# Performance work log

Measured on AMD Instinct MI355X. Metric: run time of the kernel, lower is better.

## Reference

```python
import jax, jax.numpy as jnp
import numpy as np
from jax import lax

VOCAB, EMBED, HIDDEN = 32000, 512, 1024
BATCH, SEQ = 64, 512


def setup_inputs() -> dict:
    key = jax.random.key(0)
    ks = jax.random.split(key, 10)
    H, E, V = HIDDEN, EMBED, VOCAB
    s = lambda *d: 1.0 / np.sqrt(d[0])
    return {
        "x": jax.random.randint(ks[0], (BATCH, SEQ), 0, V, dtype=jnp.int32),
        "embed_table": jax.random.normal(ks[1], (V, E), jnp.float32) * 0.02,
        "Wx0": jax.random.normal(ks[2], (E, 4 * H), jnp.float32) * s(E),
        "Wh0": jax.random.normal(ks[3], (H, 4 * H), jnp.float32) * s(H),
        "b0": jnp.zeros((4 * H,), jnp.float32),
        "Wx1": jax.random.normal(ks[4], (H, 4 * H), jnp.float32) * s(H),
        "Wh1": jax.random.normal(ks[5], (H, 4 * H), jnp.float32) * s(H),
        "b1": jnp.zeros((4 * H,), jnp.float32),
        "Wout": jax.random.normal(ks[6], (H, V), jnp.float32) * s(H),
        "bout": jnp.zeros((V,), jnp.float32),
    }


def _lstm_layer(inp, Wx, Wh, b):
    # inp: [B, S, D_in] -> hidden states [B, S, H]
    B = inp.shape[0]
    H = Wh.shape[0]
    # Precompute the input projection for all timesteps (one big GEMM).
    x4 = jnp.einsum("bsd,dg->bsg", inp, Wx) + b           # [B, S, 4H]
    x4 = jnp.swapaxes(x4, 0, 1)                              # [S, B, 4H]
    h0 = jnp.zeros((B, H), inp.dtype)
    c0 = jnp.zeros((B, H), inp.dtype)

    def step(carry, xt4):
        h, c = carry
        g = xt4 + h @ Wh                                     # [B, 4H]
        i, f, gg, o = jnp.split(g, 4, axis=-1)
        c = jax.nn.sigmoid(f) * c + jax.nn.sigmoid(i) * jnp.tanh(gg)
        h = jax.nn.sigmoid(o) * jnp.tanh(c)
        return (h, c), h

    _, hs = lax.scan(step, (h0, c0), x4)                     # hs: [S, B, H]
    return jnp.swapaxes(hs, 0, 1)                            # [B, S, H]


def reference(x, embed_table, Wx0, Wh0, b0, Wx1, Wh1, b1, Wout, bout):
    emb = embed_table[x]                                      # [B, S, E]
    h1 = _lstm_layer(emb, Wx0, Wh0, b0)                       # [B, S, H]
    h2 = _lstm_layer(h1, Wx1, Wh1, b1)                        # [B, S, H]
    logits = h2[:, -1, :] @ Wout + bout                       # [B, V] (last timestep)
    return jax.nn.softmax(logits, axis=-1)
```

## Files before the change

### kernel.cpp

```cpp
#include <hip/hip_runtime.h>


#define BB 64
#define SS 512
#define EE 512
#define HH 1024
#define GG 4096
#define VV 32000

using bf16x8 = __attribute__((ext_vector_type(8))) __bf16;
using f32x4  = __attribute__((ext_vector_type(4))) float;

__device__ __forceinline__ unsigned short f2bf(float f) {
    unsigned u = __float_as_uint(f);
    unsigned r = u + 0x7FFFu + ((u >> 16) & 1u);
    return (unsigned short)(r >> 16);
}
__device__ __forceinline__ float bf2f(unsigned short u) {
    return __uint_as_float(((unsigned)u) << 16);
}
__device__ __forceinline__ float sigm(float x) {
    return 1.0f / (1.0f + expf(-x));
}
__device__ __forceinline__ bf16x8 ld_frag_coh(const unsigned long long* p) {
    union { unsigned long long u[2]; bf16x8 v; } x;
    x.u[0] = __hip_atomic_load(p,     __ATOMIC_RELAXED, __HIP_MEMORY_SCOPE_AGENT);
    x.u[1] = __hip_atomic_load(p + 1, __ATOMIC_RELAXED, __HIP_MEMORY_SCOPE_AGENT);
    return x.v;
}
__device__ __forceinline__ void gate_poll(const unsigned int* p, unsigned tgt) {
    while (__hip_atomic_load(p, __ATOMIC_RELAXED, __HIP_MEMORY_SCOPE_AGENT) < tgt)
        __builtin_amdgcn_s_sleep(1);
    __builtin_amdgcn_sched_barrier(0);
}

__global__ void pack_b(const float* __restrict__ B, unsigned short* __restrict__ out,
                       int KT, int N) {
    int bid = blockIdx.x;
    int lane = threadIdx.x;
    int nt = bid / KT, kt = bid % KT;
    int k = kt * 32 + ((lane >> 4) << 3);
    int n = nt * 16 + (lane & 15);
    size_t base = ((size_t)bid * 64 + lane) * 8;
    #pragma unroll
    for (int j = 0; j < 8; ++j)
        out[base + j] = f2bf(B[(size_t)(k + j) * N + n]);
}

__global__ void pack_wh(const float* __restrict__ Wh, unsigned short* __restrict__ out) {
    int f = blockIdx.x;
    int lane = threadIdx.x;
    int kt = f & 31, nt = (f >> 5) & 1, g = f >> 6;
    int nloc = lane & 15;
    int q = nt * 2 + (nloc >> 3), cj = nloc & 7;
    int gcol = q * HH + 8 * g + cj;
    int k = kt * 32 + ((lane >> 4) << 3);
    size_t base = ((size_t)f * 64 + lane) * 8;
    #pragma unroll
    for (int j = 0; j < 8; ++j)
        out[base + j] = f2bf(Wh[(size_t)(k + j) * GG + gcol]);
}

__global__ void embed_pack(const int* __restrict__ x, const float* __restrict__ tab,
                           unsigned short* __restrict__ out) {
    int bid = blockIdx.x;
    int lane = threadIdx.x;
    int mt = bid >> 4, kt = bid & 15;
    int m = mt * 16 + (lane & 15);
    int idx = x[(m & 63) * SS + (m >> 6)];
    int kb = kt * 32 + ((lane >> 4) << 3);
    size_t base = ((size_t)bid * 64 + lane) * 8;
    const float* src = tab + (size_t)idx * EE + kb;
    #pragma unroll
    for (int j = 0; j < 8; ++j)
        out[base + j] = f2bf(src[j]);
}

template<int MODE>
__global__ __launch_bounds__(256) void gemm_bias(
    const unsigned short* __restrict__ Ap, const unsigned short* __restrict__ Bp,
    const float* __restrict__ bias, void* __restrict__ Cout, int N, int KT) {
    __shared__ unsigned short tile[64][72];
    const int tid = threadIdx.x, lane = tid & 63, w = tid >> 6;
    const int ntg = blockIdx.x * 4 + w;
    const int m0t = blockIdx.y * 4;
    const bf16x8* Av = reinterpret_cast<const bf16x8*>(Ap);
    const bf16x8* Bv = reinterpret_cast<const bf16x8*>(Bp);
    f32x4 acc[4] = {{0.f,0.f,0.f,0.f},{0.f,0.f,0.f,0.f},{0.f,0.f,0.f,0.f},{0.f,0.f,0.f,0.f}};
    for (int kt = 0; kt < KT; ++kt) {
        bf16x8 b = Bv[((size_t)ntg * KT + kt) * 64 + lane];
        #pragma unroll
        for (int mt = 0; mt < 4; ++mt) {
            bf16x8 a = Av[((size_t)(m0t + mt) * KT + kt) * 64 + lane];
            acc[mt] = __builtin_amdgcn_mfma_f32_16x16x32_bf16(a, b, acc[mt], 0, 0, 0);
        }
    }
    const int col = ntg * 16 + (lane & 15);
    const int rq = (lane >> 4) << 2;
    const float bb = bias[col];
    if (MODE == 0) {
        #pragma unroll
        for (int mt = 0; mt < 4; ++mt)
            #pragma unroll
            for (int i = 0; i < 4; ++i) {
                int row = (m0t + mt) * 16 + rq + i;
                ((float*)Cout)[(size_t)row * N + col] = acc[mt][i] + bb;
            }
    } else {
        const int cl = w * 16 + (lane & 15);
        #pragma unroll
        for (int mt = 0; mt < 4; ++mt)
            #pragma unroll
            for (int i = 0; i < 4; ++i)
                tile[cl][mt * 16 + rq + i] = f2bf(acc[mt][i] + bb);
        __syncthreads();
        const int c = tid >> 2, b0 = (tid & 3) << 4;
        unsigned short* dst = (unsigned short*)Cout +
            ((size_t)blockIdx.y * GG + (size_t)blockIdx.x * 64) * 64 + (size_t)tid * 16;
        const uint4* s4 = reinterpret_cast<const uint4*>(&tile[c][b0]);
        reinterpret_cast<uint4*>(dst)[0] = s4[0];
        reinterpret_cast<uint4*>(dst)[1] = s4[1];
    }
}

__global__ void zero_init(unsigned short* __restrict__ h0a,
                          unsigned short* __restrict__ h0b,
                          unsigned int* __restrict__ flags) {
    int i = blockIdx.x * 256 + threadIdx.x;
    for (int k = i; k < BB * HH; k += 64 * 256) { h0a[k] = 0; h0b[k] = 0; }
    for (int k = i; k < 9216; k += 64 * 256) flags[k] = 0;
}

__global__ __launch_bounds__(256, 2) void lstm_fused(
    const unsigned short* __restrict__ x4s,
    const unsigned short* __restrict__ wh0p, const unsigned short* __restrict__ wh1p,
    const unsigned short* __restrict__ wx1p,
    const float* __restrict__ b1,
    unsigned short* __restrict__ hb0, unsigned short* __restrict__ hb1,
    unsigned short* __restrict__ hb2, unsigned short* __restrict__ hb3,
    unsigned int* __restrict__ flags) {
    __shared__ float gx[2][32][36];
    __shared__ __align__(16) unsigned short hlds[32][8];
    __shared__ __align__(16) unsigned short Blds[64 * 64 * 8];
    const int tid = threadIdx.x, lane = tid & 63, w = tid >> 6;
    const int L = (blockIdx.x >= 256) ? 1 : 0;
    const int inner = blockIdx.x & 255;
    const int g = inner >> 1, hf = inner & 1;
    unsigned int* done   = flags + L * 4096 + hf * 2048;
    unsigned int* go_own = flags + 8192 + (L * 2 + hf) * 256;
    unsigned int* go_oth = flags + 8192 + ((1 - L) * 2 + hf) * 256;
    const int rep = (g & 15) * 16;

    {
        const uint4* src = reinterpret_cast<const uint4*>(L ? wh1p : wh0p) + (size_t)g * 4096;
        uint4* dst = reinterpret_cast<uint4*>(Blds);
        #pragma unroll
        for (int i = 0; i < 16; ++i)
            dst[i * 256 + tid] = src[i * 256 + tid];
    }
    __syncthreads();
    const bf16x8* Bl = reinterpret_cast<const bf16x8*>(Blds);
    const bf16x8* Wx = reinterpret_cast<const bf16x8*>(wx1p);

    const int msub = w & 1, kh = w >> 1;
    const int kh16 = kh * 16;
    const int nloc = lane & 15;
    const int cj = nloc & 7;
    const int q0 = nloc >> 3;
    const int gq0 = q0 * HH + 8 * g + cj;
    const int gq1 = (2 + q0) * HH + 8 * g + cj;
    const int rbase = msub * 16 + ((lane >> 4) << 2);
    const size_t afrag_base = ((size_t)(2 * hf + msub) * 32 + (size_t)kh * 16) * 64 + lane;
    const int row_l = tid >> 3, cj2 = tid & 7;
    float c = 0.f;

    if (L == 0) {
        ushort4 xv0 = {0, 0, 0, 0}, xv1 = {0, 0, 0, 0};
        if (kh == 0) {
            xv0 = *reinterpret_cast<const ushort4*>(x4s + ((size_t)gq0) * 64 + 32 * hf + rbase);
            xv1 = *reinterpret_cast<const ushort4*>(x4s + ((size_t)gq1) * 64 + 32 * hf + rbase);
        }
        #pragma unroll 1
        for (int t = 0; t < SS; ++t) {
            if (t > 0) {
                gate_poll(&go_own[rep], (unsigned)t);
                if (t >= 2) gate_poll(&go_oth[rep], (unsigned)(t - 1));
            }
            const unsigned long long* hv =
                reinterpret_cast<const unsigned long long*>((t & 1) ? hb1 : hb0);
            unsigned short* hout = (t & 1) ? hb0 : hb1;

            bf16x8 A[16];
            #pragma unroll
            for (int k = 0; k < 16; ++k)
                A[k] = ld_frag_coh(hv + (afrag_base + (size_t)k * 64) * 2);

            f32x4 acc0 = {0.f, 0.f, 0.f, 0.f}, acc1 = {0.f, 0.f, 0.f, 0.f};
            #pragma unroll
            for (int k = 0; k < 16; ++k) {
                acc0 = __builtin_amdgcn_mfma_f32_16x16x32_bf16(
                    A[k], Bl[(kh16 + k) * 64 + lane], acc0, 0, 0, 0);
                acc1 = __builtin_amdgcn_mfma_f32_16x16x32_bf16(
                    A[k], Bl[(32 + kh16 + k) * 64 + lane], acc1, 0, 0, 0);
            }
            if (kh == 0) {
                gx[0][nloc][rbase + 0] = acc0[0] + bf2f(xv0.x);
                gx[0][nloc][rbase + 1] = acc0[1] + bf2f(xv0.y);
                gx[0][nloc][rbase + 2] = acc0[2] + bf2f(xv0.z);
                gx[0][nloc][rbase + 3] = acc0[3] + bf2f(xv0.w);
                gx[0][16 + nloc][rbase + 0] = acc1[0] + bf2f(xv1.x);
                gx[0][16 + nloc][rbase + 1] = acc1[1] + bf2f(xv1.y);
                gx[0][16 + nloc][rbase + 2] = acc1[2] + bf2f(xv1.z);
                gx[0][16 + nloc][rbase + 3] = acc1[3] + bf2f(xv1.w);
            } else {
                gx[1][nloc][rbase + 0] = acc0[0];
                gx[1][nloc][rbase + 1] = acc0[1];
                gx[1][nloc][rbase + 2] = acc0[2];
                gx[1][nloc][rbase + 3] = acc0[3];
                gx[1][16 + nloc][rbase + 0] = acc1[0];
                gx[1][16 + nloc][rbase + 1] = acc1[1];
                gx[1][16 + nloc][rbase + 2] = acc1[2];
                gx[1][16 + nloc][rbase + 3] = acc1[3];
            }
            __syncthreads();

            float gi = gx[0][0 * 8 + cj2][row_l] + gx[1][0 * 8 + cj2][row_l];
            float gf = gx[0][1 * 8 + cj2][row_l] + gx[1][1 * 8 + cj2][row_l];
            float gg = gx[0][2 * 8 + cj2][row_l] + gx[1][2 * 8 + cj2][row_l];
            float go = gx[0][3 * 8 + cj2][row_l] + gx[1][3 * 8 + cj2][row_l];
            float cn = sigm(gf) * c + sigm(gi) * tanhf(gg);
            c = cn;
            hlds[row_l][cj2] = f2bf(sigm(go) * tanhf(cn));
            __syncthreads();

            if (tid < 32) {
                union { uint4 v; unsigned long long u[2]; } cv;
                cv.v = *reinterpret_cast<const uint4*>(&hlds[tid][0]);
                const int m = 32 * hf + tid;
                unsigned long long* dst = reinterpret_cast<unsigned long long*>(
                    hout + (((size_t)(m >> 4) * 32 + (g >> 2)) * 64 + (g & 3) * 16 + (m & 15)) * 8);
                __hip_atomic_store(dst,     cv.u[0], __ATOMIC_RELAXED, __HIP_MEMORY_SCOPE_AGENT);
                __hip_atomic_store(dst + 1, cv.u[1], __ATOMIC_RELAXED, __HIP_MEMORY_SCOPE_AGENT);
            }
            if (w == 0)
                asm volatile("s_waitcnt vmcnt(0)" ::: "memory");
            if (tid == 0)
                __hip_atomic_store(&done[g * 16], (unsigned)(t + 1),
                                   __ATOMIC_RELAXED, __HIP_MEMORY_SCOPE_AGENT);
            if (kh == 0 && t + 1 < SS) {
                xv0 = *reinterpret_cast<const ushort4*>(
                    x4s + ((size_t)(t + 1) * GG + gq0) * 64 + 32 * hf + rbase);
                xv1 = *reinterpret_cast<const ushort4*>(
                    x4s + ((size_t)(t + 1) * GG + gq1) * 64 + 32 * hf + rbase);
            }
            if (g == 0 && tid < 64) {
                const unsigned tgt = (unsigned)(t + 1);
                unsigned v0 = 0, v1 = 0;
                while (1) {
                    if (v0 < tgt)
                        v0 = __hip_atomic_load(&done[tid * 16], __ATOMIC_RELAXED,
                                               __HIP_MEMORY_SCOPE_AGENT);
                    if (v1 < tgt)
                        v1 = __hip_atomic_load(&done[(tid + 64) * 16], __ATOMIC_RELAXED,
                                               __HIP_MEMORY_SCOPE_AGENT);
                    if (__all((v0 >= tgt) && (v1 >= tgt))) break;
                    __builtin_amdgcn_s_sleep(1);
                }
                if (tid < 16)
                    __hip_atomic_store(&go_own[tid * 16], tgt, __ATOMIC_RELAXED,
                                       __HIP_MEMORY_SCOPE_AGENT);
            }
        }
    } else {
        const float bb0 = b1[gq0], bb1 = b1[gq1];
        #pragma unroll 1
        for (int t = 0; t < SS; ++t) {
            gate_poll(&go_oth[rep], (unsigned)(t + 1));
            const unsigned long long* hv1 =
                reinterpret_cast<const unsigned long long*>((t & 1) ? hb0 : hb1);
            bf16x8 A1[16];
            #pragma unroll
            for (int k = 0; k < 16; ++k)
                A1[k] = ld_frag_coh(hv1 + (afrag_base + (size_t)k * 64) * 2);

            if (t > 0)
                gate_poll(&go_own[rep], (unsigned)t);
            const unsigned long long* hv2 =
                reinterpret_cast<const unsigned long long*>((t & 1) ? hb3 : hb2);
            unsigned short* hout2 = (t & 1) ? hb2 : hb3;
            bf16x8 A2[16];
            #pragma unroll
            for (int k = 0; k < 16; ++k)
                A2[k] = ld_frag_coh(hv2 + (afrag_base + (size_t)k * 64) * 2);

            f32x4 acc0 = {0.f, 0.f, 0.f, 0.f}, acc1 = {0.f, 0.f, 0.f, 0.f};
            {
                bf16x8 BXa[8], BXb[8];
                #pragma unroll
                for (int j = 0; j < 8; ++j) {
                    BXa[j] = Wx[((size_t)(g * 64 + kh16 + j)) * 64 + lane];
                    BXb[j] = Wx[((size_t)(g * 64 + 32 + kh16 + j)) * 64 + lane];
                }
                #pragma unroll
                for (int j = 0; j < 8; ++j) {
                    acc0 = __builtin_amdgcn_mfma_f32_16x16x32_bf16(A1[j], BXa[j], acc0, 0, 0, 0);
                    acc1 = __builtin_amdgcn_mfma_f32_16x16x32_bf16(A1[j], BXb[j], acc1, 0, 0, 0);
                }
                #pragma unroll
                for (int j = 0; j < 8; ++j) {
                    BXa[j] = Wx[((size_t)(g * 64 + kh16 + 8 + j)) * 64 + lane];
                    BXb[j] = Wx[((size_t)(g * 64 + 32 + kh16 + 8 + j)) * 64 + lane];
                }
                #pragma unroll
                for (int j = 0; j < 8; ++j) {
                    acc0 = __builtin_amdgcn_mfma_f32_16x16x32_bf16(A1[8 + j], BXa[j], acc0, 0, 0, 0);
                    acc1 = __builtin_amdgcn_mfma_f32_16x16x32_bf16(A1[8 + j], BXb[j], acc1, 0, 0, 0);
                }
            }
            #pragma unroll
            for (int k = 0; k < 16; ++k) {
                acc0 = __builtin_amdgcn_mfma_f32_16x16x32_bf16(
                    A2[k], Bl[(kh16 + k) * 64 + lane], acc0, 0, 0, 0);
                acc1 = __builtin_amdgcn_mfma_f32_16x16x32_bf16(
                    A2[k], Bl[(32 + kh16 + k) * 64 + lane], acc1, 0, 0, 0);
            }

            if (kh == 0) {
                gx[0][nloc][rbase + 0] = acc0[0] + bb0;
                gx[0][nloc][rbase + 1] = acc0[1] + bb0;
                gx[0][nloc][rbase + 2] = acc0[2] + bb0;
                gx[0][nloc][rbase + 3] = acc0[3] + bb0;
                gx[0][16 + nloc][rbase + 0] = acc1[0] + bb1;
                gx[0][16 + nloc][rbase + 1] = acc1[1] + bb1;
                gx[0][16 + nloc][rbase + 2] = acc1[2] + bb1;
                gx[0][16 + nloc][rbase + 3] = acc1[3] + bb1;
            } else {
                gx[1][nloc][rbase + 0] = acc0[0];
                gx[1][nloc][rbase + 1] = acc0[1];
                gx[1][nloc][rbase + 2] = acc0[2];
                gx[1][nloc][rbase + 3] = acc0[3];
                gx[1][16 + nloc][rbase + 0] = acc1[0];
                gx[1][16 + nloc][rbase + 1] = acc1[1];
                gx[1][16 + nloc][rbase + 2] = acc1[2];
                gx[1][16 + nloc][rbase + 3] = acc1[3];
            }
            __syncthreads();

            float gi = gx[0][0 * 8 + cj2][row_l] + gx[1][0 * 8 + cj2][row_l];
            float gf = gx[0][1 * 8 + cj2][row_l] + gx[1][1 * 8 + cj2][row_l];
            float gg = gx[0][2 * 8 + cj2][row_l] + gx[1][2 * 8 + cj2][row_l];
            float go = gx[0][3 * 8 + cj2][row_l] + gx[1][3 * 8 + cj2][row_l];
            float cn = sigm(gf) * c + sigm(gi) * tanhf(gg);
            c = cn;
            hlds[row_l][cj2] = f2bf(sigm(go) * tanhf(cn));
            __syncthreads();

            if (tid < 32) {
                union { uint4 v; unsigned long long u[2]; } cv;
                cv.v = *reinterpret_cast<const uint4*>(&hlds[tid][0]);
                const int m = 32 * hf + tid;
                unsigned long long* dst = reinterpret_cast<unsigned long long*>(
                    hout2 + (((size_t)(m >> 4) * 32 + (g >> 2)) * 64 + (g & 3) * 16 + (m & 15)) * 8);
                __hip_atomic_store(dst,     cv.u[0], __ATOMIC_RELAXED, __HIP_MEMORY_SCOPE_AGENT);
                __hip_atomic_store(dst + 1, cv.u[1], __ATOMIC_RELAXED, __HIP_MEMORY_SCOPE_AGENT);
            }
            if (w == 0)
                asm volatile("s_waitcnt vmcnt(0)" ::: "memory");
            if (tid == 0)
                __hip_atomic_store(&done[g * 16], (unsigned)(t + 1),
                                   __ATOMIC_RELAXED, __HIP_MEMORY_SCOPE_AGENT);
            if (g == 0 && tid < 64) {
                const unsigned tgt = (unsigned)(t + 1);
                unsigned v0 = 0, v1 = 0;
                while (1) {
                    if (v0 < tgt)
                        v0 = __hip_atomic_load(&done[tid * 16], __ATOMIC_RELAXED,
                                               __HIP_MEMORY_SCOPE_AGENT);
                    if (v1 < tgt)
                        v1 = __hip_atomic_load(&done[(tid + 64) * 16], __ATOMIC_RELAXED,
                                               __HIP_MEMORY_SCOPE_AGENT);
                    if (__all((v0 >= tgt) && (v1 >= tgt))) break;
                    __builtin_amdgcn_s_sleep(1);
                }
                if (tid < 16)
                    __hip_atomic_store(&go_own[tid * 16], tgt, __ATOMIC_RELAXED,
                                       __HIP_MEMORY_SCOPE_AGENT);
            }
        }
    }
}

__global__ __launch_bounds__(256) void softmax_rows(const float* __restrict__ logits,
                                                    float* __restrict__ out) {
    __shared__ float red[256];
    int rr = blockIdx.x, tid = threadIdx.x;
    const float* L = logits + (size_t)rr * VV;
    float m = -1e30f;
    for (int i = tid; i < VV; i += 256) m = fmaxf(m, L[i]);
    red[tid] = m; __syncthreads();
    for (int s = 128; s > 0; s >>= 1) { if (tid < s) red[tid] = fmaxf(red[tid], red[tid + s]); __syncthreads(); }
    m = red[0]; __syncthreads();
    float sum = 0.f;
    for (int i = tid; i < VV; i += 256) sum += expf(L[i] - m);
    red[tid] = sum; __syncthreads();
    for (int s = 128; s > 0; s >>= 1) { if (tid < s) red[tid] += red[tid + s]; __syncthreads(); }
    float inv = 1.f / red[0];
    for (int i = tid; i < VV; i += 256) out[(size_t)rr * VV + i] = expf(L[i] - m) * inv;
}

extern "C" void kernel_launch(void* const* d_in, const int* in_sizes, int n_in,
                              void* d_out, int out_size, void* d_ws, size_t ws_size,
                              hipStream_t stream) {
    const int*   x    = (const int*)  d_in[0];
    const float* tab  = (const float*)d_in[1];
    const float* Wx0  = (const float*)d_in[2];
    const float* Wh0  = (const float*)d_in[3];
    const float* b0   = (const float*)d_in[4];
    const float* Wx1  = (const float*)d_in[5];
    const float* Wh1  = (const float*)d_in[6];
    const float* b1   = (const float*)d_in[7];
    const float* Wout = (const float*)d_in[8];
    const float* bout = (const float*)d_in[9];
    float* out = (float*)d_out;

    unsigned short* ws    = (unsigned short*)d_ws;
    unsigned short* embA  = ws;
    unsigned short* wx0p  = embA  + 16777216;
    unsigned short* wh0p  = wx0p  + 2097152;
    unsigned short* wx1p  = wh0p  + 4194304;
    unsigned short* wh1p  = wx1p  + 4194304;
    unsigned short* woutp = wh1p  + 4194304;
    unsigned short* x4s   = woutp + 32768000;
    unsigned short* h1A   = x4s   + 134217728;
    unsigned short* hb0   = h1A   + 33554432;
    unsigned short* hb1   = hb0   + 65536;
    unsigned short* hb2   = hb1   + 65536;
    unsigned short* hb3   = hb2   + 65536;
    float* logits = (float*)(hb3 + 65536);
    unsigned int* flags = (unsigned int*)(logits + 2048000);

    pack_b <<<256 * 16, 64, 0, stream>>>(Wx0, wx0p, 16, GG);
    pack_wh<<<8192, 64, 0, stream>>>(Wh0, wh0p);
    pack_wh<<<8192, 64, 0, stream>>>(Wx1, wx1p);
    pack_wh<<<8192, 64, 0, stream>>>(Wh1, wh1p);
    pack_b <<<2000 * 32, 64, 0, stream>>>(Wout, woutp, 32, VV);

    zero_init<<<64, 256, 0, stream>>>(hb0, hb2, flags);

    embed_pack<<<32768, 64, 0, stream>>>(x, tab, embA);
    gemm_bias<1><<<dim3(GG / 64, 32768 / 64), 256, 0, stream>>>(embA, wx0p, b0, x4s, GG, EE / 32);

    {
        const unsigned short* a0 = x4s;
        const unsigned short* a1 = wh0p; const unsigned short* a2 = wh1p;
        const unsigned short* a3 = wx1p; const float* a4 = b1;
        unsigned short *a5 = hb0, *a6 = hb1, *a7 = hb2, *a8 = hb3;
        unsigned int* a9 = flags;
        void* args[] = {&a0, &a1, &a2, &a3, &a4, &a5, &a6, &a7, &a8, &a9};
        hipLaunchCooperativeKernel((const void*)lstm_fused, dim3(512), dim3(256),
                                   args, 0, stream);
    }

    gemm_bias<0><<<dim3(VV / 64, 1), 256, 0, stream>>>(hb2, woutp, bout, logits, VV, HH / 32);
    softmax_rows<<<64, 256, 0, stream>>>(logits, out);
}
```

Before: 3.885 ms.

## Fuse layer-0 input projection into the recurrent LSTM kernel

Drops the separate large embedding x Wx0 GEMM and its bf16 x4s intermediate buffer. Each layer-0 block now computes its slice of the input projection per timestep inside the fused recurrent kernel, before polling for the previous hidden state. The embedding fragments for the next step are prefetched after publishing h. Wx0 is repacked into the recurrent gate layout to make this possible. This removes a large global-memory write and reread, but adds MFMA work and Wx0 global loads on every step of the serial recurrence. Hiding that work relies on it overlapping with the wait on the barrier.

```diff
diff --git a/kernel.cpp b/kernel.cpp
--- a/kernel.cpp
+++ b/kernel.cpp
@@ -47,10 +47,12 @@
         out[base + j] = f2bf(B[(size_t)(k + j) * N + n]);
 }
 
-__global__ void pack_wh(const float* __restrict__ Wh, unsigned short* __restrict__ out) {
+__global__ void pack_whk(const float* __restrict__ W, unsigned short* __restrict__ out,
+                         int KT) {
     int f = blockIdx.x;
     int lane = threadIdx.x;
-    int kt = f & 31, nt = (f >> 5) & 1, g = f >> 6;
+    int kt = f % KT, r = f / KT;
+    int nt = r & 1, g = r >> 1;
     int nloc = lane & 15;
     int q = nt * 2 + (nloc >> 3), cj = nloc & 7;
     int gcol = q * HH + 8 * g + cj;
@@ -58,7 +60,7 @@
     size_t base = ((size_t)f * 64 + lane) * 8;
     #pragma unroll
     for (int j = 0; j < 8; ++j)
-        out[base + j] = f2bf(Wh[(size_t)(k + j) * GG + gcol]);
+        out[base + j] = f2bf(W[(size_t)(k + j) * GG + gcol]);
 }
 
 __global__ void embed_pack(const int* __restrict__ x, const float* __restrict__ tab,
@@ -76,11 +78,9 @@
         out[base + j] = f2bf(src[j]);
 }
 
-template<int MODE>
 __global__ __launch_bounds__(256) void gemm_bias(
     const unsigned short* __restrict__ Ap, const unsigned short* __restrict__ Bp,
-    const float* __restrict__ bias, void* __restrict__ Cout, int N, int KT) {
-    __shared__ unsigned short tile[64][72];
+    const float* __restrict__ bias, float* __restrict__ Cout, int N, int KT) {
     const int tid = threadIdx.x, lane = tid & 63, w = tid >> 6;
     const int ntg = blockIdx.x * 4 + w;
     const int m0t = blockIdx.y * 4;
@@ -98,29 +98,13 @@
     const int col = ntg * 16 + (lane & 15);
     const int rq = (lane >> 4) << 2;
     const float bb = bias[col];
-    if (MODE == 0) {
+    #pragma unroll
+    for (int mt = 0; mt < 4; ++mt)
         #pragma unroll
-        for (int mt = 0; mt < 4; ++mt)
-            #pragma unroll
-            for (int i = 0; i < 4; ++i) {
-                int row = (m0t + mt) * 16 + rq + i;
-                ((float*)Cout)[(size_t)row * N + col] = acc[mt][i] + bb;
-            }
-    } else {
-        const int cl = w * 16 + (lane & 15);
-        #pragma unroll
-        for (int mt = 0; mt < 4; ++mt)
-            #pragma unroll
-            for (int i = 0; i < 4; ++i)
-                tile[cl][mt * 16 + rq + i] = f2bf(acc[mt][i] + bb);
-        __syncthreads();
-        const int c = tid >> 2, b0 = (tid & 3) << 4;
-        unsigned short* dst = (unsigned short*)Cout +
-            ((size_t)blockIdx.y * GG + (size_t)blockIdx.x * 64) * 64 + (size_t)tid * 16;
-        const uint4* s4 = reinterpret_cast<const uint4*>(&tile[c][b0]);
-        reinterpret_cast<uint4*>(dst)[0] = s4[0];
-        reinterpret_cast<uint4*>(dst)[1] = s4[1];
-    }
+        for (int i = 0; i < 4; ++i) {
+            int row = (m0t + mt) * 16 + rq + i;
+            Cout[(size_t)row * N + col] = acc[mt][i] + bb;
+        }
 }
 
 __global__ void zero_init(unsigned short* __restrict__ h0a,
@@ -132,10 +116,11 @@
 }
 
 __global__ __launch_bounds__(256, 2) void lstm_fused(
-    const unsigned short* __restrict__ x4s,
+    const unsigned short* __restrict__ embA,
+    const unsigned short* __restrict__ wx0p,
     const unsigned short* __restrict__ wh0p, const unsigned short* __restrict__ wh1p,
     const unsigned short* __restrict__ wx1p,
-    const float* __restrict__ b1,
+    const float* __restrict__ b0c, const float* __restrict__ b1c,
     unsigned short* __restrict__ hb0, unsigned short* __restrict__ hb1,
     unsigned short* __restrict__ hb2, unsigned short* __restrict__ hb3,
     unsigned int* __restrict__ flags) {
@@ -160,7 +145,6 @@
     }
     __syncthreads();
     const bf16x8* Bl = reinterpret_cast<const bf16x8*>(Blds);
-    const bf16x8* Wx = reinterpret_cast<const bf16x8*>(wx1p);
 
     const int msub = w & 1, kh = w >> 1;
     const int kh16 = kh * 16;
@@ -175,13 +159,27 @@
     float c = 0.f;
 
     if (L == 0) {
-        ushort4 xv0 = {0, 0, 0, 0}, xv1 = {0, 0, 0, 0};
-        if (kh == 0) {
-            xv0 = *reinterpret_cast<const ushort4*>(x4s + ((size_t)gq0) * 64 + 32 * hf + rbase);
-            xv1 = *reinterpret_cast<const ushort4*>(x4s + ((size_t)gq1) * 64 + 32 * hf + rbase);
+        const float bb0 = b0c[gq0], bb1 = b0c[gq1];
+        const bf16x8* Wx0v = reinterpret_cast<const bf16x8*>(wx0p);
+        const bf16x8* Ev   = reinterpret_cast<const bf16x8*>(embA);
+        const int kh8 = kh * 8;
+        bf16x8 Ae[8];
+        {
+            const int mt = 2 * hf + msub;
+            #pragma unroll
+            for (int j = 0; j < 8; ++j)
+                Ae[j] = Ev[((size_t)(mt * 16 + kh8 + j)) * 64 + lane];
         }
         #pragma unroll 1
         for (int t = 0; t < SS; ++t) {
+            f32x4 acc0 = {0.f, 0.f, 0.f, 0.f}, acc1 = {0.f, 0.f, 0.f, 0.f};
+            #pragma unroll
+            for (int j = 0; j < 8; ++j) {
+                bf16x8 BXa = Wx0v[((size_t)(g * 32 + kh8 + j)) * 64 + lane];
+                bf16x8 BXb = Wx0v[((size_t)(g * 32 + 16 + kh8 + j)) * 64 + lane];
+                acc0 = __builtin_amdgcn_mfma_f32_16x16x32_bf16(Ae[j], BXa, acc0, 0, 0, 0);
+                acc1 = __builtin_amdgcn_mfma_f32_16x16x32_bf16(Ae[j], BXb, acc1, 0, 0, 0);
+            }
             if (t > 0) {
                 gate_poll(&go_own[rep], (unsigned)t);
                 if (t >= 2) gate_poll(&go_oth[rep], (unsigned)(t - 1));
@@ -195,7 +193,6 @@
             for (int k = 0; k < 16; ++k)
                 A[k] = ld_frag_coh(hv + (afrag_base + (size_t)k * 64) * 2);
 
-            f32x4 acc0 = {0.f, 0.f, 0.f, 0.f}, acc1 = {0.f, 0.f, 0.f, 0.f};
             #pragma unroll
             for (int k = 0; k < 16; ++k) {
                 acc0 = __builtin_amdgcn_mfma_f32_16x16x32_bf16(
@@ -203,128 +200,6 @@
                 acc1 = __builtin_amdgcn_mfma_f32_16x16x32_bf16(
                     A[k], Bl[(32 + kh16 + k) * 64 + lane], acc1, 0, 0, 0);
             }
-            if (kh == 0) {
-                gx[0][nloc][rbase + 0] = acc0[0] + bf2f(xv0.x);
-                gx[0][nloc][rbase + 1] = acc0[1] + bf2f(xv0.y);
-                gx[0][nloc][rbase + 2] = acc0[2] + bf2f(xv0.z);
-                gx[0][nloc][rbase + 3] = acc0[3] + bf2f(xv0.w);
-                gx[0][16 + nloc][rbase + 0] = acc1[0] + bf2f(xv1.x);
-                gx[0][16 + nloc][rbase + 1] = acc1[1] + bf2f(xv1.y);
-                gx[0][16 + nloc][rbase + 2] = acc1[2] + bf2f(xv1.z);
-                gx[0][16 + nloc][rbase + 3] = acc1[3] + bf2f(xv1.w);
-            } else {
-                gx[1][nloc][rbase + 0] = acc0[0];
-                gx[1][nloc][rbase + 1] = acc0[1];
-                gx[1][nloc][rbase + 2] = acc0[2];
-                gx[1][nloc][rbase + 3] = acc0[3];
-                gx[1][16 + nloc][rbase + 0] = acc1[0];
-                gx[1][16 + nloc][rbase + 1] = acc1[1];
-                gx[1][16 + nloc][rbase + 2] = acc1[2];
-                gx[1][16 + nloc][rbase + 3] = acc1[3];
-            }
-            __syncthreads();
-
-            float gi = gx[0][0 * 8 + cj2][row_l] + gx[1][0 * 8 + cj2][row_l];
-            float gf = gx[0][1 * 8 + cj2][row_l] + gx[1][1 * 8 + cj2][row_l];
-            float gg = gx[0][2 * 8 + cj2][row_l] + gx[1][2 * 8 + cj2][row_l];
-            float go = gx[0][3 * 8 + cj2][row_l] + gx[1][3 * 8 + cj2][row_l];
-            float cn = sigm(gf) * c + sigm(gi) * tanhf(gg);
-            c = cn;
-            hlds[row_l][cj2] = f2bf(sigm(go) * tanhf(cn));
-            __syncthreads();
-
-            if (tid < 32) {
-                union { uint4 v; unsigned long long u[2]; } cv;
-                cv.v = *reinterpret_cast<const uint4*>(&hlds[tid][0]);
-                const int m = 32 * hf + tid;
-                unsigned long long* dst = reinterpret_cast<unsigned long long*>(
-                    hout + (((size_t)(m >> 4) * 32 + (g >> 2)) * 64 + (g & 3) * 16 + (m & 15)) * 8);
-                __hip_atomic_store(dst,     cv.u[0], __ATOMIC_RELAXED, __HIP_MEMORY_SCOPE_AGENT);
-                __hip_atomic_store(dst + 1, cv.u[1], __ATOMIC_RELAXED, __HIP_MEMORY_SCOPE_AGENT);
-            }
-            if (w == 0)
-                asm volatile("s_waitcnt vmcnt(0)" ::: "memory");
-            if (tid == 0)
-                __hip_atomic_store(&done[g * 16], (unsigned)(t + 1),
-                                   __ATOMIC_RELAXED, __HIP_MEMORY_SCOPE_AGENT);
-            if (kh == 0 && t + 1 < SS) {
-                xv0 = *reinterpret_cast<const ushort4*>(
-                    x4s + ((size_t)(t + 1) * GG + gq0) * 64 + 32 * hf + rbase);
-                xv1 = *reinterpret_cast<const ushort4*>(
-                    x4s + ((size_t)(t + 1) * GG + gq1) * 64 + 32 * hf + rbase);
-            }
-            if (g == 0 && tid < 64) {
-                const unsigned tgt = (unsigned)(t + 1);
-                unsigned v0 = 0, v1 = 0;
-                while (1) {
-                    if (v0 < tgt)
-                        v0 = __hip_atomic_load(&done[tid * 16], __ATOMIC_RELAXED,
-                                               __HIP_MEMORY_SCOPE_AGENT);
-                    if (v1 < tgt)
-                        v1 = __hip_atomic_load(&done[(tid + 64) * 16], __ATOMIC_RELAXED,
-                                               __HIP_MEMORY_SCOPE_AGENT);
-                    if (__all((v0 >= tgt) && (v1 >= tgt))) break;
-                    __builtin_amdgcn_s_sleep(1);
-                }
-                if (tid < 16)
-                    __hip_atomic_store(&go_own[tid * 16], tgt, __ATOMIC_RELAXED,
-                                       __HIP_MEMORY_SCOPE_AGENT);
-            }
-        }
-    } else {
-        const float bb0 = b1[gq0], bb1 = b1[gq1];
-        #pragma unroll 1
-        for (int t = 0; t < SS; ++t) {
-            gate_poll(&go_oth[rep], (unsigned)(t + 1));
-            const unsigned long long* hv1 =
-                reinterpret_cast<const unsigned long long*>((t & 1) ? hb0 : hb1);
-            bf16x8 A1[16];
-            #pragma unroll
-            for (int k = 0; k < 16; ++k)
-                A1[k] = ld_frag_coh(hv1 + (afrag_base + (size_t)k * 64) * 2);
-
-            if (t > 0)
-                gate_poll(&go_own[rep], (unsigned)t);
-            const unsigned long long* hv2 =
-                reinterpret_cast<const unsigned long long*>((t & 1) ? hb3 : hb2);
-            unsigned short* hout2 = (t & 1) ? hb2 : hb3;
-            bf16x8 A2[16];
-            #pragma unroll
-            for (int k = 0; k < 16; ++k)
-                A2[k] = ld_frag_coh(hv2 + (afrag_base + (size_t)k * 64) * 2);
-
-            f32x4 acc0 = {0.f, 0.f, 0.f, 0.f}, acc1 = {0.f, 0.f, 0.f, 0.f};
-            {
-                bf16x8 BXa[8], BXb[8];
-                #pragma unroll
-                for (int j = 0; j < 8; ++j) {
-                    BXa[j] = Wx[((size_t)(g * 64 + kh16 + j)) * 64 + lane];
-                    BXb[j] = Wx[((size_t)(g * 64 + 32 + kh16 + j)) * 64 + lane];
-                }
-                #pragma unroll
-                for (int j = 0; j < 8; ++j) {
-                    acc0 = __builtin_amdgcn_mfma_f32_16x16x32_bf16(A1[j], BXa[j], acc0, 0, 0, 0);
-                    acc1 = __builtin_amdgcn_mfma_f32_16x16x32_bf16(A1[j], BXb[j], acc1, 0, 0, 0);
-                }
-                #pragma unroll
-                for (int j = 0; j < 8; ++j) {
-                    BXa[j] = Wx[((size_t)(g * 64 + kh16 + 8 + j)) * 64 + lane];
-                    BXb[j] = Wx[((size_t)(g * 64 + 32 + kh16 + 8 + j)) * 64 + lane];
-                }
-                #pragma unroll
-                for (int j = 0; j < 8; ++j) {
-                    acc0 = __builtin_amdgcn_mfma_f32_16x16x32_bf16(A1[8 + j], BXa[j], acc0, 0, 0, 0);
-                    acc1 = __builtin_amdgcn_mfma_f32_16x16x32_bf16(A1[8 + j], BXb[j], acc1, 0, 0, 0);
-                }
-            }
-            #pragma unroll
-            for (int k = 0; k < 16; ++k) {
-                acc0 = __builtin_amdgcn_mfma_f32_16x16x32_bf16(
-                    A2[k], Bl[(kh16 + k) * 64 + lane], acc0, 0, 0, 0);
-                acc1 = __builtin_amdgcn_mfma_f32_16x16x32_bf16(
-                    A2[k], Bl[(32 + kh16 + k) * 64 + lane], acc1, 0, 0, 0);
-            }
-
             if (kh == 0) {
                 gx[0][nloc][rbase + 0] = acc0[0] + bb0;
                 gx[0][nloc][rbase + 1] = acc0[1] + bb0;
@@ -360,6 +235,129 @@
                 cv.v = *reinterpret_cast<const uint4*>(&hlds[tid][0]);
                 const int m = 32 * hf + tid;
                 unsigned long long* dst = reinterpret_cast<unsigned long long*>(
+                    hout + (((size_t)(m >> 4) * 32 + (g >> 2)) * 64 + (g & 3) * 16 + (m & 15)) * 8);
+                __hip_atomic_store(dst,     cv.u[0], __ATOMIC_RELAXED, __HIP_MEMORY_SCOPE_AGENT);
+                __hip_atomic_store(dst + 1, cv.u[1], __ATOMIC_RELAXED, __HIP_MEMORY_SCOPE_AGENT);
+            }
+            if (w == 0)
+                asm volatile("s_waitcnt vmcnt(0)" ::: "memory");
+            if (tid == 0)
+                __hip_atomic_store(&done[g * 16], (unsigned)(t + 1),
+                                   __ATOMIC_RELAXED, __HIP_MEMORY_SCOPE_AGENT);
+            if (t + 1 < SS) {
+                const int mt1 = 4 * (t + 1) + 2 * hf + msub;
+                #pragma unroll
+                for (int j = 0; j < 8; ++j)
+                    Ae[j] = Ev[((size_t)(mt1 * 16 + kh8 + j)) * 64 + lane];
+            }
+            if (g == 0 && tid < 64) {
+                const unsigned tgt = (unsigned)(t + 1);
+                unsigned v0 = 0, v1 = 0;
+                while (1) {
+                    if (v0 < tgt)
+                        v0 = __hip_atomic_load(&done[tid * 16], __ATOMIC_RELAXED,
+                                               __HIP_MEMORY_SCOPE_AGENT);
+                    if (v1 < tgt)
+                        v1 = __hip_atomic_load(&done[(tid + 64) * 16], __ATOMIC_RELAXED,
+                                               __HIP_MEMORY_SCOPE_AGENT);
+                    if (__all((v0 >= tgt) && (v1 >= tgt))) break;
+                    __builtin_amdgcn_s_sleep(1);
+                }
+                if (tid < 16)
+                    __hip_atomic_store(&go_own[tid * 16], tgt, __ATOMIC_RELAXED,
+                                       __HIP_MEMORY_SCOPE_AGENT);
+            }
+        }
+    } else {
+        const float bb0 = b1c[gq0], bb1 = b1c[gq1];
+        const bf16x8* Wx = reinterpret_cast<const bf16x8*>(wx1p);
+        #pragma unroll 1
+        for (int t = 0; t < SS; ++t) {
+            gate_poll(&go_oth[rep], (unsigned)(t + 1));
+            const unsigned long long* hv1 =
+                reinterpret_cast<const unsigned long long*>((t & 1) ? hb0 : hb1);
+            bf16x8 A1[16];
+            #pragma unroll
+            for (int k = 0; k < 16; ++k)
+                A1[k] = ld_frag_coh(hv1 + (afrag_base + (size_t)k * 64) * 2);
+
+            if (t > 0)
+                gate_poll(&go_own[rep], (unsigned)t);
+            const unsigned long long* hv2 =
+                reinterpret_cast<const unsigned long long*>((t & 1) ? hb3 : hb2);
+            unsigned short* hout2 = (t & 1) ? hb2 : hb3;
+            bf16x8 A2[16];
+            #pragma unroll
+            for (int k = 0; k < 16; ++k)
+                A2[k] = ld_frag_coh(hv2 + (afrag_base + (size_t)k * 64) * 2);
+
+            f32x4 acc0 = {0.f, 0.f, 0.f, 0.f}, acc1 = {0.f, 0.f, 0.f, 0.f};
+            {
+                bf16x8 BXa[8], BXb[8];
+                #pragma unroll
+                for (int j = 0; j < 8; ++j) {
+                    BXa[j] = Wx[((size_t)(g * 64 + kh16 + j)) * 64 + lane];
+                    BXb[j] = Wx[((size_t)(g * 64 + 32 + kh16 + j)) * 64 + lane];
+                }
+                #pragma unroll
+                for (int j = 0; j < 8; ++j) {
+                    acc0 = __builtin_amdgcn_mfma_f32_16x16x32_bf16(A1[j], BXa[j], acc0, 0, 0, 0);
+                    acc1 = __builtin_amdgcn_mfma_f32_16x16x32_bf16(A1[j], BXb[j], acc1, 0, 0, 0);
+                }
+                #pragma unroll
+                for (int j = 0; j < 8; ++j) {
+                    BXa[j] = Wx[((size_t)(g * 64 + kh16 + 8 + j)) * 64 + lane];
+                    BXb[j] = Wx[((size_t)(g * 64 + 32 + kh16 + 8 + j)) * 64 + lane];
+                }
+                #pragma unroll
+                for (int j = 0; j < 8; ++j) {
+                    acc0 = __builtin_amdgcn_mfma_f32_16x16x32_bf16(A1[8 + j], BXa[j], acc0, 0, 0, 0);
+                    acc1 = __builtin_amdgcn_mfma_f32_16x16x32_bf16(A1[8 + j], BXb[j], acc1, 0, 0, 0);
+                }
+            }
+            #pragma unroll
+            for (int k = 0; k < 16; ++k) {
+                acc0 = __builtin_amdgcn_mfma_f32_16x16x32_bf16(
+                    A2[k], Bl[(kh16 + k) * 64 + lane], acc0, 0, 0, 0);
+                acc1 = __builtin_amdgcn_mfma_f32_16x16x32_bf16(
+                    A2[k], Bl[(32 + kh16 + k) * 64 + lane], acc1, 0, 0, 0);
+            }
+
+            if (kh == 0) {
+                gx[0][nloc][rbase + 0] = acc0[0] + bb0;
+                gx[0][nloc][rbase + 1] = acc0[1] + bb0;
+                gx[0][nloc][rbase + 2] = acc0[2] + bb0;
+                gx[0][nloc][rbase + 3] = acc0[3] + bb0;
+                gx[0][16 + nloc][rbase + 0] = acc1[0] + bb1;
+                gx[0][16 + nloc][rbase + 1] = acc1[1] + bb1;
+                gx[0][16 + nloc][rbase + 2] = acc1[2] + bb1;
+                gx[0][16 + nloc][rbase + 3] = acc1[3] + bb1;
+            } else {
+                gx[1][nloc][rbase + 0] = acc0[0];
+                gx[1][nloc][rbase + 1] = acc0[1];
+                gx[1][nloc][rbase + 2] = acc0[2];
+                gx[1][nloc][rbase + 3] = acc0[3];
+                gx[1][16 + nloc][rbase + 0] = acc1[0];
+                gx[1][16 + nloc][rbase + 1] = acc1[1];
+                gx[1][16 + nloc][rbase + 2] = acc1[2];
+                gx[1][16 + nloc][rbase + 3] = acc1[3];
+            }
+            __syncthreads();
+
+            float gi = gx[0][0 * 8 + cj2][row_l] + gx[1][0 * 8 + cj2][row_l];
+            float gf = gx[0][1 * 8 + cj2][row_l] + gx[1][1 * 8 + cj2][row_l];
+            float gg = gx[0][2 * 8 + cj2][row_l] + gx[1][2 * 8 + cj2][row_l];
+            float go = gx[0][3 * 8 + cj2][row_l] + gx[1][3 * 8 + cj2][row_l];
+            float cn = sigm(gf) * c + sigm(gi) * tanhf(gg);
+            c = cn;
+            hlds[row_l][cj2] = f2bf(sigm(go) * tanhf(cn));
+            __syncthreads();
+
+            if (tid < 32) {
+                union { uint4 v; unsigned long long u[2]; } cv;
+                cv.v = *reinterpret_cast<const uint4*>(&hlds[tid][0]);
+                const int m = 32 * hf + tid;
+                unsigned long long* dst = reinterpret_cast<unsigned long long*>(
                     hout2 + (((size_t)(m >> 4) * 32 + (g >> 2)) * 64 + (g & 3) * 16 + (m & 15)) * 8);
                 __hip_atomic_store(dst,     cv.u[0], __ATOMIC_RELAXED, __HIP_MEMORY_SCOPE_AGENT);
                 __hip_atomic_store(dst + 1, cv.u[1], __ATOMIC_RELAXED, __HIP_MEMORY_SCOPE_AGENT);
@@ -430,37 +428,35 @@
     unsigned short* wx1p  = wh0p  + 4194304;
     unsigned short* wh1p  = wx1p  + 4194304;
     unsigned short* woutp = wh1p  + 4194304;
-    unsigned short* x4s   = woutp + 32768000;
-    unsigned short* h1A   = x4s   + 134217728;
-    unsigned short* hb0   = h1A   + 33554432;
+    unsigned short* hb0   = woutp + 32768000;
     unsigned short* hb1   = hb0   + 65536;
     unsigned short* hb2   = hb1   + 65536;
     unsigned short* hb3   = hb2   + 65536;
     float* logits = (float*)(hb3 + 65536);
     unsigned int* flags = (unsigned int*)(logits + 2048000);
 
-    pack_b <<<256 * 16, 64, 0, stream>>>(Wx0, wx0p, 16, GG);
-    pack_wh<<<8192, 64, 0, stream>>>(Wh0, wh0p);
-    pack_wh<<<8192, 64, 0, stream>>>(Wx1, wx1p);
-    pack_wh<<<8192, 64, 0, stream>>>(Wh1, wh1p);
+    pack_whk<<<4096, 64, 0, stream>>>(Wx0, wx0p, 16);
+    pack_whk<<<8192, 64, 0, stream>>>(Wh0, wh0p, 32);
+    pack_whk<<<8192, 64, 0, stream>>>(Wx1, wx1p, 32);
+    pack_whk<<<8192, 64, 0, stream>>>(Wh1, wh1p, 32);
     pack_b <<<2000 * 32, 64, 0, stream>>>(Wout, woutp, 32, VV);
 
     zero_init<<<64, 256, 0, stream>>>(hb0, hb2, flags);
 
     embed_pack<<<32768, 64, 0, stream>>>(x, tab, embA);
-    gemm_bias<1><<<dim3(GG / 64, 32768 / 64), 256, 0, stream>>>(embA, wx0p, b0, x4s, GG, EE / 32);
 
     {
-        const unsigned short* a0 = x4s;
-        const unsigned short* a1 = wh0p; const unsigned short* a2 = wh1p;
-        const unsigned short* a3 = wx1p; const float* a4 = b1;
-        unsigned short *a5 = hb0, *a6 = hb1, *a7 = hb2, *a8 = hb3;
-        unsigned int* a9 = flags;
-        void* args[] = {&a0, &a1, &a2, &a3, &a4, &a5, &a6, &a7, &a8, &a9};
+        const unsigned short* a0 = embA; const unsigned short* a1 = wx0p;
+        const unsigned short* a2 = wh0p; const unsigned short* a3 = wh1p;
+        const unsigned short* a4 = wx1p;
+        const float* a5 = b0; const float* a6 = b1;
+        unsigned short *a7 = hb0, *a8 = hb1, *a9 = hb2, *a10 = hb3;
+        unsigned int* a11 = flags;
+        void* args[] = {&a0, &a1, &a2, &a3, &a4, &a5, &a6, &a7, &a8, &a9, &a10, &a11};
         hipLaunchCooperativeKernel((const void*)lstm_fused, dim3(512), dim3(256),
                                    args, 0, stream);
     }
 
-    gemm_bias<0><<<dim3(VV / 64, 1), 256, 0, stream>>>(hb2, woutp, bout, logits, VV, HH / 32);
+    gemm_bias<<<dim3(VV / 64, 1), 256, 0, stream>>>(hb2, woutp, bout, logits, VV, HH / 32);
     softmax_rows<<<64, 256, 0, stream>>>(logits, out);
 }
```

Result: faster. 3.531 ms (-9.1%).
